# Kernel tuning notes

Hardware: AMD Instinct MI355X
Metric: run time of the kernel (lower is better)

The kernel has to match this reference:

```python
import jax, jax.numpy as jnp
import numpy as np

B, C, H, W = 8, 512, 32, 32
HEADS = 8
GROUPS = 32
EPS = 1e-5


def setup_inputs() -> dict:
    key = jax.random.key(0)
    ks = jax.random.split(key, 7)
    x = jax.random.normal(ks[0], (B, C, H, W), dtype=jnp.float32)
    gamma = jnp.ones((C,), dtype=jnp.float32)
    beta = jnp.zeros((C,), dtype=jnp.float32)
    w_qkv = jax.random.normal(ks[1], (3 * C, C), dtype=jnp.float32) * 0.02
    b_qkv = jnp.zeros((3 * C,), dtype=jnp.float32)
    # NOTE: original zero-inits proj; we use small random weights so the
    # attention path contributes to the output (zero proj => out == x).
    w_proj = jax.random.normal(ks[2], (C, C), dtype=jnp.float32) * 0.02
    b_proj = jnp.zeros((C,), dtype=jnp.float32)
    return {"x": x, "gamma": gamma, "beta": beta, "w_qkv": w_qkv,
            "b_qkv": b_qkv, "w_proj": w_proj, "b_proj": b_proj}


def group_norm(x, gamma, beta):
    b, c, h, w = x.shape
    xg = x.reshape(b, GROUPS, -1)
    mu = xg.mean(axis=-1, keepdims=True)
    var = xg.var(axis=-1, keepdims=True)
    xn = ((xg - mu) * jax.lax.rsqrt(var + EPS)).reshape(b, c, h, w)
    return xn * gamma[:, None, None] + beta[:, None, None]


def reference(x, gamma, beta, w_qkv, b_qkv, w_proj, b_proj):
    b, c, h, w = x.shape
    hd = c // HEADS
    n = h * w
    hn = group_norm(x, gamma, beta).reshape(b, c, n)        # [B,C,N]
    # 1x1 conv == channel matmul
    qkv = jnp.einsum('oc,bcn->bon', w_qkv, hn) + b_qkv[:, None]
    qkv = qkv.reshape(b, 3, HEADS, hd, n)
    q, k, v = qkv[:, 0], qkv[:, 1], qkv[:, 2]               # [B,H,hd,N]
    scale = hd ** -0.5
    scores = jnp.einsum('bhci,bhcj->bhij', q, k) * scale    # [B,H,N,N]
    attn = jax.nn.softmax(scores, axis=-1)                  # stable (max-sub)
    out = jnp.einsum('bhij,bhcj->bhci', attn, v).reshape(b, c, n)
    proj = jnp.einsum('oc,bcn->bon', w_proj, out) + b_proj[:, None]
    return x + proj.reshape(b, c, h, w)
```

## Files before the change

### kernel.cpp

```cpp
#include <hip/hip_runtime.h>
#include <math.h>

#define Bn 8
#define Cc 512
#define HW 1024
#define HEADS 8
#define HD 64
#define GROUPS 32
#define CPG 16
#define EPS 1e-5f

typedef float f32x4 __attribute__((ext_vector_type(4)));
typedef __bf16 bf16x8 __attribute__((ext_vector_type(8)));
typedef __bf16 bf16x4 __attribute__((ext_vector_type(4)));
typedef short s16x4 __attribute__((ext_vector_type(4)));
typedef unsigned u32x2 __attribute__((ext_vector_type(2)));

__device__ __forceinline__ void async16(const __bf16* g, __bf16* l) {
    __builtin_amdgcn_global_load_lds((const __attribute__((address_space(1))) unsigned int*)g,
                                     (__attribute__((address_space(3))) unsigned int*)l, 16, 0, 0);
}

__device__ __forceinline__ f32x4 mfma16(bf16x4 a, bf16x4 b, f32x4 c) {
    return __builtin_amdgcn_mfma_f32_16x16x16bf16_1k(
        __builtin_bit_cast(s16x4, a), __builtin_bit_cast(s16x4, b), c, 0, 0, 0);
}

__device__ __forceinline__ unsigned pk_bf16(float f1, float f0) {
    return __builtin_amdgcn_perm(__builtin_bit_cast(unsigned, f1),
                                 __builtin_bit_cast(unsigned, f0), 0x07060302u);
}

__global__ __launch_bounds__(256) void gn_fused(const float* __restrict__ x,
                                                const float* __restrict__ gamma,
                                                const float* __restrict__ beta,
                                                __bf16* __restrict__ hnT,
                                                const float* __restrict__ wq,
                                                __bf16* __restrict__ wq_bf,
                                                const float* __restrict__ wp,
                                                __bf16* __restrict__ wp_bf) {
    int blk = blockIdx.x;
    int tid = threadIdx.x;
    if (blk >= 256) {
        int i = (blk - 256) * 256 + tid;
        if (i < 196608) {
            float4 v = ((const float4*)wq)[i];
            bf16x4 o = { (__bf16)v.x, (__bf16)v.y, (__bf16)v.z, (__bf16)v.w };
            ((bf16x4*)wq_bf)[i] = o;
        } else {
            int j = i - 196608;
            float4 v = ((const float4*)wp)[j];
            bf16x4 o = { (__bf16)v.x, (__bf16)v.y, (__bf16)v.z, (__bf16)v.w };
            ((bf16x4*)wp_bf)[j] = o;
        }
        return;
    }
    int b = blk >> 5, g = blk & 31;
    const float* xp = x + ((size_t)b * Cc + g * CPG) * HW;

    __shared__ __align__(16) __bf16 xs[16 * 1024];
    __shared__ float red0[4], red1[4];
    __shared__ float gls[16], bls[16], stats[2];
    if (tid < 16) { gls[tid] = gamma[g * CPG + tid]; bls[tid] = beta[g * CPG + tid]; }

    float s = 0.f, ss = 0.f;
    for (int i4 = tid; i4 < 4096; i4 += 256) {
        float4 v = ((const float4*)xp)[i4];
        s  += (v.x + v.y) + (v.z + v.w);
        ss += (v.x * v.x + v.y * v.y) + (v.z * v.z + v.w * v.w);
        bf16x4 o = { (__bf16)v.x, (__bf16)v.y, (__bf16)v.z, (__bf16)v.w };
        ((bf16x4*)xs)[i4] = o;
    }
    for (int off = 32; off > 0; off >>= 1) {
        s  += __shfl_down(s, off);
        ss += __shfl_down(ss, off);
    }
    int wave = tid >> 6, lane = tid & 63;
    if (lane == 0) { red0[wave] = s; red1[wave] = ss; }
    __syncthreads();
    if (tid == 0) {
        float S  = red0[0] + red0[1] + red0[2] + red0[3];
        float SS = red1[0] + red1[1] + red1[2] + red1[3];
        float mean = S / (float)(CPG * HW);
        float var  = SS / (float)(CPG * HW) - mean * mean;
        stats[0] = mean;
        stats[1] = rsqrtf(var + EPS);
    }
    __syncthreads();
    float mean = stats[0], rstd = stats[1];
    #pragma unroll
    for (int u = 0; u < 4; ++u) {
        int n = tid + u * 256;
        union { __bf16 bs[16]; uint4 q[2]; } o;
        #pragma unroll
        for (int c = 0; c < 16; ++c) {
            float v = (float)xs[c * 1024 + n];
            o.bs[c] = (__bf16)((v - mean) * rstd * gls[c] + bls[c]);
        }
        uint4* dst = (uint4*)(hnT + ((size_t)b * HW + n) * Cc + g * CPG);
        dst[0] = o.q[0];
        dst[1] = o.q[1];
    }
}

__global__ __launch_bounds__(256) void qkv_gemm(
    const __bf16* __restrict__ hnT, const __bf16* __restrict__ wq,
    const float* __restrict__ bias, __bf16* __restrict__ qkT,
    __bf16* __restrict__ vbuf, float scaleLo) {
    __shared__ __align__(16) __bf16 As[128 * 64];
    __shared__ __align__(16) __bf16 Bs[128 * 64];
    int tid = threadIdx.x;
    int wv = tid >> 6, lane = tid & 63, ln = lane & 15, quad = lane >> 4;
    int b = blockIdx.z;
    bool isQK = blockIdx.y < 8;
    int bm = (isQK ? blockIdx.y : blockIdx.y - 8) * 128;
    int bn = blockIdx.x * 128;
    const __bf16* hb = hnT + (size_t)b * HW * Cc;
    const __bf16* Pb = isQK ? hb : wq + (size_t)1024 * 512;
    const __bf16* Qb = isQK ? wq : hb;
    int wm = (wv >> 1) * 64, wn = (wv & 1) * 64;

    f32x4 acc[4][4];
    #pragma unroll
    for (int i = 0; i < 4; ++i)
        #pragma unroll
        for (int j = 0; j < 4; ++j) acc[i][j] = (f32x4){0.f, 0.f, 0.f, 0.f};

    for (int k0 = 0; k0 < 512; k0 += 64) {
        __syncthreads();
        #pragma unroll
        for (int u = 0; u < 4; ++u) {
            int idx = u * 256 + tid;
            int r = idx >> 3, lc = idx & 7;
            int cg = lc ^ (r & 7);
            async16(Pb + (size_t)(bm + r) * 512 + k0 + cg * 8, &As[r * 64 + lc * 8]);
            async16(Qb + (size_t)(bn + r) * 512 + k0 + cg * 8, &Bs[r * 64 + lc * 8]);
        }
        __syncthreads();
        bf16x8 af[4][2], bff[4][2];
        #pragma unroll
        for (int mt = 0; mt < 4; ++mt) {
            int row = wm + mt * 16 + ln;
            #pragma unroll
            for (int h = 0; h < 2; ++h) {
                int cc = (h * 4 + quad) ^ (ln & 7);
                af[mt][h] = *(const bf16x8*)&As[row * 64 + cc * 8];
            }
        }
        #pragma unroll
        for (int nt = 0; nt < 4; ++nt) {
            int row = wn + nt * 16 + ln;
            #pragma unroll
            for (int h = 0; h < 2; ++h) {
                int cc = (h * 4 + quad) ^ (ln & 7);
                bff[nt][h] = *(const bf16x8*)&Bs[row * 64 + cc * 8];
            }
        }
        #pragma unroll
        for (int mt = 0; mt < 4; ++mt)
            #pragma unroll
            for (int nt = 0; nt < 4; ++nt) {
                acc[mt][nt] = __builtin_amdgcn_mfma_f32_16x16x32_bf16(af[mt][0], bff[nt][0], acc[mt][nt], 0, 0, 0);
                acc[mt][nt] = __builtin_amdgcn_mfma_f32_16x16x32_bf16(af[mt][1], bff[nt][1], acc[mt][nt], 0, 0, 0);
            }
    }

    if (isQK) {
        __bf16* out = qkT + (size_t)b * HW * 1024;
        float bcol[4], scol[4];
        #pragma unroll
        for (int nt = 0; nt < 4; ++nt) {
            int col = bn + wn + nt * 16 + ln;
            bcol[nt] = bias[col];
            scol[nt] = (col < 512) ? scaleLo : 1.0f;
        }
        #pragma unroll
        for (int mt = 0; mt < 4; ++mt)
            #pragma unroll
            for (int r = 0; r < 4; ++r) {
                int row = bm + wm + mt * 16 + quad * 4 + r;
                #pragma unroll
                for (int nt = 0; nt < 4; ++nt) {
                    int col = bn + wn + nt * 16 + ln;
                    out[(size_t)row * 1024 + col] = (__bf16)((acc[mt][nt][r] + bcol[nt]) * scol[nt]);
                }
            }
    } else {
        __bf16* out = vbuf + (size_t)b * Cc * HW;
        #pragma unroll
        for (int mt = 0; mt < 4; ++mt)
            #pragma unroll
            for (int r = 0; r < 4; ++r) {
                int row = bm + wm + mt * 16 + quad * 4 + r;
                float brow = bias[1024 + row];
                #pragma unroll
                for (int nt = 0; nt < 4; ++nt) {
                    int col = bn + wn + nt * 16 + ln;
                    out[(size_t)row * 1024 + col] = (__bf16)(acc[mt][nt][r] + brow);
                }
            }
    }
}

__global__ __launch_bounds__(256) void proj_gemm(
    const __bf16* __restrict__ wp, const __bf16* __restrict__ attnT,
    const float* __restrict__ bias, const float* __restrict__ resid,
    float* __restrict__ outp) {
    __shared__ __align__(16) __bf16 As[64 * 64];
    __shared__ __align__(16) __bf16 Bs[128 * 64];
    int tid = threadIdx.x;
    int wv = tid >> 6, lane = tid & 63, ln = lane & 15, quad = lane >> 4;
    int b = blockIdx.z;
    int bm = blockIdx.y * 64, bn = blockIdx.x * 128;
    const __bf16* Qb = attnT + (size_t)b * HW * Cc;
    int wm = (wv >> 1) * 32, wn = (wv & 1) * 64;

    f32x4 acc[2][4];
    #pragma unroll
    for (int i = 0; i < 2; ++i)
        #pragma unroll
        for (int j = 0; j < 4; ++j) acc[i][j] = (f32x4){0.f, 0.f, 0.f, 0.f};

    for (int k0 = 0; k0 < 512; k0 += 64) {
        __syncthreads();
        #pragma unroll
        for (int u = 0; u < 2; ++u) {
            int idx = u * 256 + tid;
            int r = idx >> 3, lc = idx & 7;
            int cg = lc ^ (r & 7);
            async16(wp + (size_t)(bm + r) * 512 + k0 + cg * 8, &As[r * 64 + lc * 8]);
        }
        #pragma unroll
        for (int u = 0; u < 4; ++u) {
            int idx = u * 256 + tid;
            int r = idx >> 3, lc = idx & 7;
            int cg = lc ^ (r & 7);
            async16(Qb + (size_t)(bn + r) * 512 + k0 + cg * 8, &Bs[r * 64 + lc * 8]);
        }
        __syncthreads();
        bf16x8 af[2][2], bff[4][2];
        #pragma unroll
        for (int mt = 0; mt < 2; ++mt) {
            int row = wm + mt * 16 + ln;
            #pragma unroll
            for (int h = 0; h < 2; ++h) {
                int cc = (h * 4 + quad) ^ (ln & 7);
                af[mt][h] = *(const bf16x8*)&As[row * 64 + cc * 8];
            }
        }
        #pragma unroll
        for (int nt = 0; nt < 4; ++nt) {
            int row = wn + nt * 16 + ln;
            #pragma unroll
            for (int h = 0; h < 2; ++h) {
                int cc = (h * 4 + quad) ^ (ln & 7);
                bff[nt][h] = *(const bf16x8*)&Bs[row * 64 + cc * 8];
            }
        }
        #pragma unroll
        for (int mt = 0; mt < 2; ++mt)
            #pragma unroll
            for (int nt = 0; nt < 4; ++nt) {
                acc[mt][nt] = __builtin_amdgcn_mfma_f32_16x16x32_bf16(af[mt][0], bff[nt][0], acc[mt][nt], 0, 0, 0);
                acc[mt][nt] = __builtin_amdgcn_mfma_f32_16x16x32_bf16(af[mt][1], bff[nt][1], acc[mt][nt], 0, 0, 0);
            }
    }

    float* out = outp + (size_t)b * Cc * HW;
    const float* res = resid + (size_t)b * Cc * HW;
    #pragma unroll
    for (int mt = 0; mt < 2; ++mt)
        #pragma unroll
        for (int r = 0; r < 4; ++r) {
            int row = bm + wm + mt * 16 + quad * 4 + r;
            float bv = bias[row];
            #pragma unroll
            for (int nt = 0; nt < 4; ++nt) {
                int col = bn + wn + nt * 16 + ln;
                size_t idx = (size_t)row * 1024 + col;
                out[idx] = acc[mt][nt][r] + bv + res[idx];
            }
        }
}

__global__ __launch_bounds__(256) void attn_mfma(const __bf16* __restrict__ qkT,
                                                 const __bf16* __restrict__ vbuf,
                                                 __bf16* __restrict__ attnT) {
    __shared__ __align__(16) __bf16 Ks[2][64 * 64];
    __shared__ __align__(16) __bf16 Vs[2][64 * 64];
    int tid = threadIdx.x;
    int wv = tid >> 6, lane = tid & 63, ln = lane & 15, quad = lane >> 4;
    int h = blockIdx.x, b = blockIdx.z;
    int i0 = blockIdx.y * 128 + wv * 32;

    const __bf16* qbase = qkT + ((size_t)b * HW + i0 + ln) * 1024 + h * HD + quad * 8;
    bf16x8 qf[2][2];
    #pragma unroll
    for (int mt = 0; mt < 2; ++mt) {
        qf[mt][0] = *(const bf16x8*)(qbase + (size_t)mt * 16 * 1024);
        qf[mt][1] = *(const bf16x8*)(qbase + (size_t)mt * 16 * 1024 + 32);
    }

    f32x4 oacc[2][4];
    #pragma unroll
    for (int mt = 0; mt < 2; ++mt)
        #pragma unroll
        for (int ct = 0; ct < 4; ++ct) oacc[mt][ct] = (f32x4){0.f, 0.f, 0.f, 0.f};
    float lsum[2] = {0.f, 0.f};

    for (int kt = 0; kt < 8; ++kt) {
        __syncthreads();
        #pragma unroll
        for (int hh = 0; hh < 2; ++hh) {
            int kb = kt * 128 + hh * 64;
            #pragma unroll
            for (int u = 0; u < 2; ++u) {
                int idx = u * 256 + tid;
                int r = idx >> 3, lc = idx & 7;
                int cg = lc ^ (r & 7);
                async16(qkT + ((size_t)b * HW + kb + r) * 1024 + 512 + h * HD + cg * 8,
                        &Ks[hh][idx * 8]);
                async16(vbuf + ((size_t)b * Cc + h * HD + r) * HW + kb + cg * 8,
                        &Vs[hh][idx * 8]);
            }
        }
        __syncthreads();

        #pragma unroll
        for (int hh = 0; hh < 2; ++hh) {
            f32x4 st[2][4];
            #pragma unroll
            for (int jt = 0; jt < 4; ++jt) {
                int row = jt * 16 + ln;
                int c0 = quad ^ (ln & 7);
                int c1 = (4 + quad) ^ (ln & 7);
                bf16x8 kf0 = *(const bf16x8*)&Ks[hh][row * 64 + c0 * 8];
                bf16x8 kf1 = *(const bf16x8*)&Ks[hh][row * 64 + c1 * 8];
                #pragma unroll
                for (int mt = 0; mt < 2; ++mt) {
                    f32x4 s = (f32x4){0.f, 0.f, 0.f, 0.f};
                    s = __builtin_amdgcn_mfma_f32_16x16x32_bf16(kf0, qf[mt][0], s, 0, 0, 0);
                    s = __builtin_amdgcn_mfma_f32_16x16x32_bf16(kf1, qf[mt][1], s, 0, 0, 0);
                    st[mt][jt] = s;
                }
            }

            bf16x4 pk[2][4];
            #pragma unroll
            for (int mt = 0; mt < 2; ++mt)
                #pragma unroll
                for (int jt = 0; jt < 4; ++jt) {
                    float p0 = __builtin_amdgcn_exp2f(st[mt][jt][0]);
                    float p1 = __builtin_amdgcn_exp2f(st[mt][jt][1]);
                    float p2 = __builtin_amdgcn_exp2f(st[mt][jt][2]);
                    float p3 = __builtin_amdgcn_exp2f(st[mt][jt][3]);
                    lsum[mt] += (p0 + p1) + (p2 + p3);
                    u32x2 w = { pk_bf16(p1, p0), pk_bf16(p3, p2) };
                    pk[mt][jt] = __builtin_bit_cast(bf16x4, w);
                }

            #pragma unroll
            for (int ct = 0; ct < 4; ++ct) {
                int row = ct * 16 + ln;
                bf16x4 vf[4];
                #pragma unroll
                for (int kss = 0; kss < 4; ++kss) {
                    int cc16 = (kss * 2 + (quad >> 1)) ^ (ln & 7);
                    vf[kss] = *(const bf16x4*)&Vs[hh][row * 64 + cc16 * 8 + (quad & 1) * 4];
                }
                #pragma unroll
                for (int mt = 0; mt < 2; ++mt)
                    #pragma unroll
                    for (int kss = 0; kss < 4; ++kss)
                        oacc[mt][ct] = mfma16(vf[kss], pk[mt][kss], oacc[mt][ct]);
            }
        }
    }

    #pragma unroll
    for (int mt = 0; mt < 2; ++mt) {
        lsum[mt] += __shfl_xor(lsum[mt], 16);
        lsum[mt] += __shfl_xor(lsum[mt], 32);
        float rl = 1.f / lsum[mt];
        __bf16* op = attnT + ((size_t)b * HW + i0 + mt * 16 + ln) * Cc + h * HD + quad * 4;
        #pragma unroll
        for (int ct = 0; ct < 4; ++ct) {
            bf16x4 o = { (__bf16)(oacc[mt][ct][0] * rl), (__bf16)(oacc[mt][ct][1] * rl),
                         (__bf16)(oacc[mt][ct][2] * rl), (__bf16)(oacc[mt][ct][3] * rl) };
            *(bf16x4*)(op + ct * 16) = o;
        }
    }
}

extern "C" void kernel_launch(void* const* d_in, const int* in_sizes, int n_in,
                              void* d_out, int out_size, void* d_ws, size_t ws_size,
                              hipStream_t stream) {
    const float* x      = (const float*)d_in[0];
    const float* gamma  = (const float*)d_in[1];
    const float* beta   = (const float*)d_in[2];
    const float* w_qkv  = (const float*)d_in[3];
    const float* b_qkv  = (const float*)d_in[4];
    const float* w_proj = (const float*)d_in[5];
    const float* b_proj = (const float*)d_in[6];
    float* out = (float*)d_out;

    __bf16* wq_bf  = (__bf16*)d_ws;
    __bf16* wp_bf  = wq_bf + (size_t)1536 * 512;
    __bf16* hnT    = wp_bf + (size_t)512 * 512;
    __bf16* qkT    = hnT + (size_t)Bn * HW * Cc;
    __bf16* vbuf   = qkT + (size_t)Bn * HW * 1024;
    __bf16* attnT  = vbuf + (size_t)Bn * Cc * HW;

    gn_fused<<<1280, 256, 0, stream>>>(x, gamma, beta, hnT, w_qkv, wq_bf, w_proj, wp_bf);

    const float QSCALE = 0.125f * 1.44269504088896f;
    dim3 gqkv(8, 12, Bn);
    qkv_gemm<<<gqkv, 256, 0, stream>>>(hnT, wq_bf, b_qkv, qkT, vbuf, QSCALE);

    dim3 ga(8, 8, 8);
    attn_mfma<<<ga, 256, 0, stream>>>(qkT, vbuf, attnT);

    dim3 gp(8, 8, Bn);
    proj_gemm<<<gp, 256, 0, stream>>>(wp_bf, attnT, b_proj, x, out);
}
```

Baseline: 146.0 us.

## Fuse all four stages into one cooperative persistent kernel with grid syncs

Merges group norm, QKV GEMM, attention and projection into a single cooperative kernel of 512 blocks that separates stages with grid-wide barriers. This removes kernel launch gaps and tail effects between stages, and it falls back to four separate launches if cooperative launch is unavailable. Shared memory is cut to a common 32KB buffer, which means group norm reuses the bf16 staging area for its reductions and now reads gamma and beta straight from global memory. The grid barriers add their own cost, the QKV stage now loops over 768 tiles on 512 blocks and so runs unevenly, and the occupancy hint may raise register pressure.

```diff
diff --git a/kernel.cpp b/kernel.cpp
--- a/kernel.cpp
+++ b/kernel.cpp
@@ -1,5 +1,8 @@
 #include <hip/hip_runtime.h>
+#include <hip/hip_cooperative_groups.h>
 #include <math.h>
+
+namespace cg = cooperative_groups;
 
 #define Bn 8
 #define Cc 512
@@ -31,37 +34,33 @@
                                  __builtin_bit_cast(unsigned, f0), 0x07060302u);
 }
 
-__global__ __launch_bounds__(256) void gn_fused(const float* __restrict__ x,
-                                                const float* __restrict__ gamma,
-                                                const float* __restrict__ beta,
-                                                __bf16* __restrict__ hnT,
-                                                const float* __restrict__ wq,
-                                                __bf16* __restrict__ wq_bf,
-                                                const float* __restrict__ wp,
-                                                __bf16* __restrict__ wp_bf) {
-    int blk = blockIdx.x;
-    int tid = threadIdx.x;
+__device__ __forceinline__ void gn_phase(char* smem, int blk, int tid,
+    const float* __restrict__ x, const float* __restrict__ gamma,
+    const float* __restrict__ beta, __bf16* __restrict__ hnT,
+    const float* __restrict__ wq, __bf16* __restrict__ wq_bf,
+    const float* __restrict__ wp, __bf16* __restrict__ wp_bf) {
     if (blk >= 256) {
-        int i = (blk - 256) * 256 + tid;
-        if (i < 196608) {
-            float4 v = ((const float4*)wq)[i];
-            bf16x4 o = { (__bf16)v.x, (__bf16)v.y, (__bf16)v.z, (__bf16)v.w };
-            ((bf16x4*)wq_bf)[i] = o;
-        } else {
-            int j = i - 196608;
-            float4 v = ((const float4*)wp)[j];
-            bf16x4 o = { (__bf16)v.x, (__bf16)v.y, (__bf16)v.z, (__bf16)v.w };
-            ((bf16x4*)wp_bf)[j] = o;
+        int base = (blk - 256) * 1024 + tid;
+        #pragma unroll
+        for (int u = 0; u < 4; ++u) {
+            int i = base + u * 256;
+            if (i < 196608) {
+                float4 v = ((const float4*)wq)[i];
+                bf16x4 o = { (__bf16)v.x, (__bf16)v.y, (__bf16)v.z, (__bf16)v.w };
+                ((bf16x4*)wq_bf)[i] = o;
+            } else {
+                int j = i - 196608;
+                float4 v = ((const float4*)wp)[j];
+                bf16x4 o = { (__bf16)v.x, (__bf16)v.y, (__bf16)v.z, (__bf16)v.w };
+                ((bf16x4*)wp_bf)[j] = o;
+            }
         }
         return;
     }
+    __bf16* xs = (__bf16*)smem;
+    float* fs = (float*)smem;
     int b = blk >> 5, g = blk & 31;
     const float* xp = x + ((size_t)b * Cc + g * CPG) * HW;
-
-    __shared__ __align__(16) __bf16 xs[16 * 1024];
-    __shared__ float red0[4], red1[4];
-    __shared__ float gls[16], bls[16], stats[2];
-    if (tid < 16) { gls[tid] = gamma[g * CPG + tid]; bls[tid] = beta[g * CPG + tid]; }
 
     float s = 0.f, ss = 0.f;
     for (int i4 = tid; i4 < 4096; i4 += 256) {
@@ -76,18 +75,29 @@
         ss += __shfl_down(ss, off);
     }
     int wave = tid >> 6, lane = tid & 63;
-    if (lane == 0) { red0[wave] = s; red1[wave] = ss; }
+    __syncthreads();
+    float keep = 0.f;
+    if (tid < 20) keep = (float)xs[tid];
+    __syncthreads();
+    if (lane == 0) { fs[wave * 2] = s; fs[wave * 2 + 1] = ss; }
     __syncthreads();
     if (tid == 0) {
-        float S  = red0[0] + red0[1] + red0[2] + red0[3];
-        float SS = red1[0] + red1[1] + red1[2] + red1[3];
-        float mean = S / (float)(CPG * HW);
-        float var  = SS / (float)(CPG * HW) - mean * mean;
-        stats[0] = mean;
-        stats[1] = rsqrtf(var + EPS);
-    }
-    __syncthreads();
-    float mean = stats[0], rstd = stats[1];
+        float S  = fs[0] + fs[2] + fs[4] + fs[6];
+        float SS = fs[1] + fs[3] + fs[5] + fs[7];
+        float mean = S / 16384.f;
+        float var  = SS / 16384.f - mean * mean;
+        fs[8] = mean;
+        fs[9] = rsqrtf(var + EPS);
+    }
+    __syncthreads();
+    float mean = fs[8], rstd = fs[9];
+    __syncthreads();
+    if (tid < 20) xs[tid] = (__bf16)keep;
+    __syncthreads();
+
+    float gl[16], bl[16];
+    #pragma unroll
+    for (int c = 0; c < 16; ++c) { gl[c] = gamma[g * CPG + c]; bl[c] = beta[g * CPG + c]; }
     #pragma unroll
     for (int u = 0; u < 4; ++u) {
         int n = tid + u * 256;
@@ -95,7 +105,7 @@
         #pragma unroll
         for (int c = 0; c < 16; ++c) {
             float v = (float)xs[c * 1024 + n];
-            o.bs[c] = (__bf16)((v - mean) * rstd * gls[c] + bls[c]);
+            o.bs[c] = (__bf16)((v - mean) * rstd * gl[c] + bl[c]);
         }
         uint4* dst = (uint4*)(hnT + ((size_t)b * HW + n) * Cc + g * CPG);
         dst[0] = o.q[0];
@@ -103,18 +113,18 @@
     }
 }
 
-__global__ __launch_bounds__(256) void qkv_gemm(
+__device__ __forceinline__ void qkv_tile(char* smem, int t, int tid,
     const __bf16* __restrict__ hnT, const __bf16* __restrict__ wq,
     const float* __restrict__ bias, __bf16* __restrict__ qkT,
     __bf16* __restrict__ vbuf, float scaleLo) {
-    __shared__ __align__(16) __bf16 As[128 * 64];
-    __shared__ __align__(16) __bf16 Bs[128 * 64];
-    int tid = threadIdx.x;
+    __bf16* As = (__bf16*)smem;
+    __bf16* Bs = (__bf16*)(smem + 16384);
     int wv = tid >> 6, lane = tid & 63, ln = lane & 15, quad = lane >> 4;
-    int b = blockIdx.z;
-    bool isQK = blockIdx.y < 8;
-    int bm = (isQK ? blockIdx.y : blockIdx.y - 8) * 128;
-    int bn = blockIdx.x * 128;
+    int b = t / 96, rem = t % 96;
+    int y = rem >> 3, xv = rem & 7;
+    bool isQK = y < 8;
+    int bm = (isQK ? y : y - 8) * 128;
+    int bn = xv * 128;
     const __bf16* hb = hnT + (size_t)b * HW * Cc;
     const __bf16* Pb = isQK ? hb : wq + (size_t)1024 * 512;
     const __bf16* Qb = isQK ? wq : hb;
@@ -132,9 +142,9 @@
         for (int u = 0; u < 4; ++u) {
             int idx = u * 256 + tid;
             int r = idx >> 3, lc = idx & 7;
-            int cg = lc ^ (r & 7);
-            async16(Pb + (size_t)(bm + r) * 512 + k0 + cg * 8, &As[r * 64 + lc * 8]);
-            async16(Qb + (size_t)(bn + r) * 512 + k0 + cg * 8, &Bs[r * 64 + lc * 8]);
+            int cg2 = lc ^ (r & 7);
+            async16(Pb + (size_t)(bm + r) * 512 + k0 + cg2 * 8, &As[r * 64 + lc * 8]);
+            async16(Qb + (size_t)(bn + r) * 512 + k0 + cg2 * 8, &Bs[r * 64 + lc * 8]);
         }
         __syncthreads();
         bf16x8 af[4][2], bff[4][2];
@@ -202,96 +212,14 @@
     }
 }
 
-__global__ __launch_bounds__(256) void proj_gemm(
-    const __bf16* __restrict__ wp, const __bf16* __restrict__ attnT,
-    const float* __restrict__ bias, const float* __restrict__ resid,
-    float* __restrict__ outp) {
-    __shared__ __align__(16) __bf16 As[64 * 64];
-    __shared__ __align__(16) __bf16 Bs[128 * 64];
-    int tid = threadIdx.x;
+__device__ __forceinline__ void attn_unit(char* smem, int blk, int tid,
+    const __bf16* __restrict__ qkT, const __bf16* __restrict__ vbuf,
+    __bf16* __restrict__ attnT) {
+    __bf16* Ks = (__bf16*)smem;
+    __bf16* Vs = (__bf16*)(smem + 16384);
     int wv = tid >> 6, lane = tid & 63, ln = lane & 15, quad = lane >> 4;
-    int b = blockIdx.z;
-    int bm = blockIdx.y * 64, bn = blockIdx.x * 128;
-    const __bf16* Qb = attnT + (size_t)b * HW * Cc;
-    int wm = (wv >> 1) * 32, wn = (wv & 1) * 64;
-
-    f32x4 acc[2][4];
-    #pragma unroll
-    for (int i = 0; i < 2; ++i)
-        #pragma unroll
-        for (int j = 0; j < 4; ++j) acc[i][j] = (f32x4){0.f, 0.f, 0.f, 0.f};
-
-    for (int k0 = 0; k0 < 512; k0 += 64) {
-        __syncthreads();
-        #pragma unroll
-        for (int u = 0; u < 2; ++u) {
-            int idx = u * 256 + tid;
-            int r = idx >> 3, lc = idx & 7;
-            int cg = lc ^ (r & 7);
-            async16(wp + (size_t)(bm + r) * 512 + k0 + cg * 8, &As[r * 64 + lc * 8]);
-        }
-        #pragma unroll
-        for (int u = 0; u < 4; ++u) {
-            int idx = u * 256 + tid;
-            int r = idx >> 3, lc = idx & 7;
-            int cg = lc ^ (r & 7);
-            async16(Qb + (size_t)(bn + r) * 512 + k0 + cg * 8, &Bs[r * 64 + lc * 8]);
-        }
-        __syncthreads();
-        bf16x8 af[2][2], bff[4][2];
-        #pragma unroll
-        for (int mt = 0; mt < 2; ++mt) {
-            int row = wm + mt * 16 + ln;
-            #pragma unroll
-            for (int h = 0; h < 2; ++h) {
-                int cc = (h * 4 + quad) ^ (ln & 7);
-                af[mt][h] = *(const bf16x8*)&As[row * 64 + cc * 8];
-            }
-        }
-        #pragma unroll
-        for (int nt = 0; nt < 4; ++nt) {
-            int row = wn + nt * 16 + ln;
-            #pragma unroll
-            for (int h = 0; h < 2; ++h) {
-                int cc = (h * 4 + quad) ^ (ln & 7);
-                bff[nt][h] = *(const bf16x8*)&Bs[row * 64 + cc * 8];
-            }
-        }
-        #pragma unroll
-        for (int mt = 0; mt < 2; ++mt)
-            #pragma unroll
-            for (int nt = 0; nt < 4; ++nt) {
-                acc[mt][nt] = __builtin_amdgcn_mfma_f32_16x16x32_bf16(af[mt][0], bff[nt][0], acc[mt][nt], 0, 0, 0);
-                acc[mt][nt] = __builtin_amdgcn_mfma_f32_16x16x32_bf16(af[mt][1], bff[nt][1], acc[mt][nt], 0, 0, 0);
-            }
-    }
-
-    float* out = outp + (size_t)b * Cc * HW;
-    const float* res = resid + (size_t)b * Cc * HW;
-    #pragma unroll
-    for (int mt = 0; mt < 2; ++mt)
-        #pragma unroll
-        for (int r = 0; r < 4; ++r) {
-            int row = bm + wm + mt * 16 + quad * 4 + r;
-            float bv = bias[row];
-            #pragma unroll
-            for (int nt = 0; nt < 4; ++nt) {
-                int col = bn + wn + nt * 16 + ln;
-                size_t idx = (size_t)row * 1024 + col;
-                out[idx] = acc[mt][nt][r] + bv + res[idx];
-            }
-        }
-}
-
-__global__ __launch_bounds__(256) void attn_mfma(const __bf16* __restrict__ qkT,
-                                                 const __bf16* __restrict__ vbuf,
-                                                 __bf16* __restrict__ attnT) {
-    __shared__ __align__(16) __bf16 Ks[2][64 * 64];
-    __shared__ __align__(16) __bf16 Vs[2][64 * 64];
-    int tid = threadIdx.x;
-    int wv = tid >> 6, lane = tid & 63, ln = lane & 15, quad = lane >> 4;
-    int h = blockIdx.x, b = blockIdx.z;
-    int i0 = blockIdx.y * 128 + wv * 32;
+    int h = blk & 7, qb = (blk >> 3) & 7, b = blk >> 6;
+    int i0 = qb * 128 + wv * 32;
 
     const __bf16* qbase = qkT + ((size_t)b * HW + i0 + ln) * 1024 + h * HD + quad * 8;
     bf16x8 qf[2][2];
@@ -317,11 +245,11 @@
             for (int u = 0; u < 2; ++u) {
                 int idx = u * 256 + tid;
                 int r = idx >> 3, lc = idx & 7;
-                int cg = lc ^ (r & 7);
-                async16(qkT + ((size_t)b * HW + kb + r) * 1024 + 512 + h * HD + cg * 8,
-                        &Ks[hh][idx * 8]);
-                async16(vbuf + ((size_t)b * Cc + h * HD + r) * HW + kb + cg * 8,
-                        &Vs[hh][idx * 8]);
+                int cg2 = lc ^ (r & 7);
+                async16(qkT + ((size_t)b * HW + kb + r) * 1024 + 512 + h * HD + cg2 * 8,
+                        &Ks[hh * 4096 + idx * 8]);
+                async16(vbuf + ((size_t)b * Cc + h * HD + r) * HW + kb + cg2 * 8,
+                        &Vs[hh * 4096 + idx * 8]);
             }
         }
         __syncthreads();
@@ -334,8 +262,8 @@
                 int row = jt * 16 + ln;
                 int c0 = quad ^ (ln & 7);
                 int c1 = (4 + quad) ^ (ln & 7);
-                bf16x8 kf0 = *(const bf16x8*)&Ks[hh][row * 64 + c0 * 8];
-                bf16x8 kf1 = *(const bf16x8*)&Ks[hh][row * 64 + c1 * 8];
+                bf16x8 kf0 = *(const bf16x8*)&Ks[hh * 4096 + row * 64 + c0 * 8];
+                bf16x8 kf1 = *(const bf16x8*)&Ks[hh * 4096 + row * 64 + c1 * 8];
                 #pragma unroll
                 for (int mt = 0; mt < 2; ++mt) {
                     f32x4 s = (f32x4){0.f, 0.f, 0.f, 0.f};
@@ -366,7 +294,7 @@
                 #pragma unroll
                 for (int kss = 0; kss < 4; ++kss) {
                     int cc16 = (kss * 2 + (quad >> 1)) ^ (ln & 7);
-                    vf[kss] = *(const bf16x4*)&Vs[hh][row * 64 + cc16 * 8 + (quad & 1) * 4];
+                    vf[kss] = *(const bf16x4*)&Vs[hh * 4096 + row * 64 + cc16 * 8 + (quad & 1) * 4];
                 }
                 #pragma unroll
                 for (int mt = 0; mt < 2; ++mt)
@@ -390,6 +318,131 @@
             *(bf16x4*)(op + ct * 16) = o;
         }
     }
+}
+
+__device__ __forceinline__ void proj_unit(char* smem, int blk, int tid,
+    const __bf16* __restrict__ wp, const __bf16* __restrict__ attnT,
+    const float* __restrict__ bias, const float* __restrict__ resid,
+    float* __restrict__ outp) {
+    __bf16* As = (__bf16*)smem;
+    __bf16* Bs = (__bf16*)(smem + 8192);
+    int wv = tid >> 6, lane = tid & 63, ln = lane & 15, quad = lane >> 4;
+    int xv = blk & 7, y = (blk >> 3) & 7, b = blk >> 6;
+    int bm = y * 64, bn = xv * 128;
+    const __bf16* Qb = attnT + (size_t)b * HW * Cc;
+    int wm = (wv >> 1) * 32, wn = (wv & 1) * 64;
+
+    f32x4 acc[2][4];
+    #pragma unroll
+    for (int i = 0; i < 2; ++i)
+        #pragma unroll
+        for (int j = 0; j < 4; ++j) acc[i][j] = (f32x4){0.f, 0.f, 0.f, 0.f};
+
+    for (int k0 = 0; k0 < 512; k0 += 64) {
+        __syncthreads();
+        #pragma unroll
+        for (int u = 0; u < 2; ++u) {
+            int idx = u * 256 + tid;
+            int r = idx >> 3, lc = idx & 7;
+            int cg2 = lc ^ (r & 7);
+            async16(wp + (size_t)(bm + r) * 512 + k0 + cg2 * 8, &As[r * 64 + lc * 8]);
+        }
+        #pragma unroll
+        for (int u = 0; u < 4; ++u) {
+            int idx = u * 256 + tid;
+            int r = idx >> 3, lc = idx & 7;
+            int cg2 = lc ^ (r & 7);
+            async16(Qb + (size_t)(bn + r) * 512 + k0 + cg2 * 8, &Bs[r * 64 + lc * 8]);
+        }
+        __syncthreads();
+        bf16x8 af[2][2], bff[4][2];
+        #pragma unroll
+        for (int mt = 0; mt < 2; ++mt) {
+            int row = wm + mt * 16 + ln;
+            #pragma unroll
+            for (int h = 0; h < 2; ++h) {
+                int cc = (h * 4 + quad) ^ (ln & 7);
+                af[mt][h] = *(const bf16x8*)&As[row * 64 + cc * 8];
+            }
+        }
+        #pragma unroll
+        for (int nt = 0; nt < 4; ++nt) {
+            int row = wn + nt * 16 + ln;
+            #pragma unroll
+            for (int h = 0; h < 2; ++h) {
+                int cc = (h * 4 + quad) ^ (ln & 7);
+                bff[nt][h] = *(const bf16x8*)&Bs[row * 64 + cc * 8];
+            }
+        }
+        #pragma unroll
+        for (int mt = 0; mt < 2; ++mt)
+            #pragma unroll
+            for (int nt = 0; nt < 4; ++nt) {
+                acc[mt][nt] = __builtin_amdgcn_mfma_f32_16x16x32_bf16(af[mt][0], bff[nt][0], acc[mt][nt], 0, 0, 0);
+                acc[mt][nt] = __builtin_amdgcn_mfma_f32_16x16x32_bf16(af[mt][1], bff[nt][1], acc[mt][nt], 0, 0, 0);
+            }
+    }
+
+    float* out = outp + (size_t)b * Cc * HW;
+    const float* res = resid + (size_t)b * Cc * HW;
+    #pragma unroll
+    for (int mt = 0; mt < 2; ++mt)
+        #pragma unroll
+        for (int r = 0; r < 4; ++r) {
+            int row = bm + wm + mt * 16 + quad * 4 + r;
+            float bv = bias[row];
+            #pragma unroll
+            for (int nt = 0; nt < 4; ++nt) {
+                int col = bn + wn + nt * 16 + ln;
+                size_t idx = (size_t)row * 1024 + col;
+                out[idx] = acc[mt][nt][r] + bv + res[idx];
+            }
+        }
+}
+
+__global__ __launch_bounds__(256, 2) void mega(
+    const float* __restrict__ x, const float* __restrict__ gamma,
+    const float* __restrict__ beta,
+    const float* __restrict__ wq_f, const float* __restrict__ wp_f,
+    const float* __restrict__ bq, const float* __restrict__ bp,
+    __bf16* wq_bf, __bf16* wp_bf, __bf16* hnT, __bf16* qkT,
+    __bf16* vbuf, __bf16* attnT, float* out, float qscale) {
+    __shared__ __align__(16) char smem[32768];
+    int blk = blockIdx.x, tid = threadIdx.x;
+    cg::grid_group grid = cg::this_grid();
+
+    gn_phase(smem, blk, tid, x, gamma, beta, hnT, wq_f, wq_bf, wp_f, wp_bf);
+    grid.sync();
+    for (int t = blk; t < 768; t += 512)
+        qkv_tile(smem, t, tid, hnT, wq_bf, bq, qkT, vbuf, qscale);
+    grid.sync();
+    attn_unit(smem, blk, tid, qkT, vbuf, attnT);
+    grid.sync();
+    proj_unit(smem, blk, tid, wp_bf, attnT, bp, x, out);
+}
+
+__global__ __launch_bounds__(256, 2) void gn_k(
+    const float* x, const float* gamma, const float* beta, __bf16* hnT,
+    const float* wq, __bf16* wq_bf, const float* wp, __bf16* wp_bf) {
+    __shared__ __align__(16) char smem[32768];
+    gn_phase(smem, blockIdx.x, threadIdx.x, x, gamma, beta, hnT, wq, wq_bf, wp, wp_bf);
+}
+__global__ __launch_bounds__(256, 2) void qkv_k(
+    const __bf16* hnT, const __bf16* wq, const float* bq,
+    __bf16* qkT, __bf16* vbuf, float qscale) {
+    __shared__ __align__(16) char smem[32768];
+    qkv_tile(smem, blockIdx.x, threadIdx.x, hnT, wq, bq, qkT, vbuf, qscale);
+}
+__global__ __launch_bounds__(256, 2) void attn_k(
+    const __bf16* qkT, const __bf16* vbuf, __bf16* attnT) {
+    __shared__ __align__(16) char smem[32768];
+    attn_unit(smem, blockIdx.x, threadIdx.x, qkT, vbuf, attnT);
+}
+__global__ __launch_bounds__(256, 2) void proj_k(
+    const __bf16* wp, const __bf16* attnT, const float* bp,
+    const float* resid, float* out) {
+    __shared__ __align__(16) char smem[32768];
+    proj_unit(smem, blockIdx.x, threadIdx.x, wp, attnT, bp, resid, out);
 }
 
 extern "C" void kernel_launch(void* const* d_in, const int* in_sizes, int n_in,
@@ -411,15 +464,29 @@
     __bf16* vbuf   = qkT + (size_t)Bn * HW * 1024;
     __bf16* attnT  = vbuf + (size_t)Bn * Cc * HW;
 
-    gn_fused<<<1280, 256, 0, stream>>>(x, gamma, beta, hnT, w_qkv, wq_bf, w_proj, wp_bf);
-
-    const float QSCALE = 0.125f * 1.44269504088896f;
-    dim3 gqkv(8, 12, Bn);
-    qkv_gemm<<<gqkv, 256, 0, stream>>>(hnT, wq_bf, b_qkv, qkT, vbuf, QSCALE);
-
-    dim3 ga(8, 8, 8);
-    attn_mfma<<<ga, 256, 0, stream>>>(qkT, vbuf, attnT);
-
-    dim3 gp(8, 8, Bn);
-    proj_gemm<<<gp, 256, 0, stream>>>(wp_bf, attnT, b_proj, x, out);
-}
+    float qscale = 0.125f * 1.44269504088896f;
+
+    int dev = 0;
+    hipGetDevice(&dev);
+    int coop = 0, ncu = 0, maxBlk = 0;
+    hipDeviceGetAttribute(&coop, hipDeviceAttributeCooperativeLaunch, dev);
+    hipDeviceGetAttribute(&ncu, hipDeviceAttributeMultiprocessorCount, dev);
+    hipOccupancyMaxActiveBlocksPerMultiprocessor(&maxBlk, mega, 256, 0);
+    bool useCoop = coop && ((long)maxBlk * (long)ncu >= 512);
+
+    hipError_t err = hipErrorUnknown;
+    if (useCoop) {
+        void* args[] = { (void*)&x, (void*)&gamma, (void*)&beta,
+                         (void*)&w_qkv, (void*)&w_proj, (void*)&b_qkv, (void*)&b_proj,
+                         (void*)&wq_bf, (void*)&wp_bf, (void*)&hnT, (void*)&qkT,
+                         (void*)&vbuf, (void*)&attnT, (void*)&out, (void*)&qscale };
+        err = hipLaunchCooperativeKernel((const void*)mega, dim3(512), dim3(256),
+                                         args, 0, stream);
+    }
+    if (err != hipSuccess) {
+        gn_k<<<512, 256, 0, stream>>>(x, gamma, beta, hnT, w_qkv, wq_bf, w_proj, wp_bf);
+        qkv_k<<<768, 256, 0, stream>>>(hnT, wq_bf, b_qkv, qkT, vbuf, qscale);
+        attn_k<<<512, 256, 0, stream>>>(qkT, vbuf, attnT);
+        proj_k<<<512, 256, 0, stream>>>(wp_bf, attnT, b_proj, x, out);
+    }
+}
```

Result: faster. 136.2 us (-6.7%).
